# Performance work log

Measured on AMD Instinct MI355X. Metric: run time of the kernel, lower is better.

## Reference

```python
import jax, jax.numpy as jnp
import numpy as np

B, T, C, H = 4, 2048, 1024, 16
HS = C // H          # 64
DFF = 4 * C          # 4096
EPS = 1e-5


def _layernorm(x, g, b):
    mu = jnp.mean(x, axis=-1, keepdims=True)
    var = jnp.mean(jnp.square(x - mu), axis=-1, keepdims=True)
    return (x - mu) * jax.lax.rsqrt(var + EPS) * g + b


def setup_inputs() -> dict:
    key = jax.random.key(0)
    ks = jax.random.split(key, 12)
    s = 0.02
    return {
        "x": jax.random.normal(ks[0], (B, T, C), jnp.float32),
        "Wq": jax.random.normal(ks[1], (H, C, HS), jnp.float32) * s,
        "Wk": jax.random.normal(ks[2], (H, C, HS), jnp.float32) * s,
        "Wv": jax.random.normal(ks[3], (H, C, HS), jnp.float32) * s,
        "Wproj": jax.random.normal(ks[4], (C, C), jnp.float32) * s,
        "bproj": jnp.zeros((C,), jnp.float32),
        "ln1_g": jnp.ones((C,), jnp.float32),
        "ln1_b": jnp.zeros((C,), jnp.float32),
        "ln2_g": jnp.ones((C,), jnp.float32),
        "ln2_b": jnp.zeros((C,), jnp.float32),
        "W1": jax.random.normal(ks[5], (C, DFF), jnp.float32) * s,
        "b1": jnp.zeros((DFF,), jnp.float32),
        "W2": jax.random.normal(ks[6], (DFF, C), jnp.float32) * s,
        "b2": jnp.zeros((C,), jnp.float32),
    }


def reference(x, Wq, Wk, Wv, Wproj, bproj, ln1_g, ln1_b, ln2_g, ln2_b, W1, b1, W2, b2):
    Tn = x.shape[1]
    Cn = x.shape[2]
    # --- self-attention on ln1(x) ---
    h = _layernorm(x, ln1_g, ln1_b)
    q = jnp.einsum('btc,hcd->bhtd', h, Wq)
    k = jnp.einsum('btc,hcd->bhtd', h, Wk)
    v = jnp.einsum('btc,hcd->bhtd', h, Wv)
    # NOTE: original scales by C**-0.5 (full embed dim), not head_size**-0.5
    scores = jnp.einsum('bhtd,bhsd->bhts', q, k) * (Cn ** -0.5)
    mask = jnp.tril(jnp.ones((Tn, Tn), dtype=bool))
    scores = jnp.where(mask, scores, jnp.float32(-jnp.inf))
    att = jax.nn.softmax(scores, axis=-1)
    o = jnp.einsum('bhts,bhsd->bhtd', att, v)          # [B,H,T,HS]
    o = o.transpose(0, 2, 1, 3).reshape(x.shape)       # concat heads -> [B,T,C]
    x = x + o @ Wproj + bproj
    # --- feed-forward on ln2(x) ---
    h2 = _layernorm(x, ln2_g, ln2_b)
    x = x + jax.nn.relu(h2 @ W1 + b1) @ W2 + b2
    return x
```

## Files before the change

### kernel.cpp

```cpp
#include <hip/hip_runtime.h>
#include <hip/hip_bf16.h>
#include <stdint.h>

typedef __attribute__((ext_vector_type(8))) __bf16 bf16x8;
typedef __attribute__((ext_vector_type(4))) __bf16 bf16x4;
typedef __attribute__((ext_vector_type(4))) float f32x4;
typedef __attribute__((ext_vector_type(16))) float f32x16;
typedef __attribute__((ext_vector_type(4))) unsigned int u32x4;

typedef const __attribute__((address_space(1))) void* gas_ptr;
typedef __attribute__((address_space(3))) void* las_ptr;

static __device__ __forceinline__ void gload_lds16(const void* g, void* l) {
  __builtin_amdgcn_global_load_lds((gas_ptr)g, (las_ptr)l, 16, 0, 0);
}

static __device__ __forceinline__ unsigned int cvt_pk(float lo, float hi) {
  unsigned int r;
  asm("v_cvt_pk_bf16_f32 %0, %1, %2" : "=v"(r) : "v"(lo), "v"(hi));
  return r;
}

static __device__ __forceinline__ bf16x8 pack_frag(unsigned int a, unsigned int b,
                                                   unsigned int c, unsigned int d) {
  u32x4 t = {a, b, c, d};
  return __builtin_bit_cast(bf16x8, t);
}

static __device__ __forceinline__ void vm4() {
  asm volatile("s_waitcnt vmcnt(4)" ::: "memory");
}
static __device__ __forceinline__ void vm0() {
  asm volatile("s_waitcnt vmcnt(0)" ::: "memory");
}
static __device__ __forceinline__ void lgkm0sb() {
  asm volatile("s_waitcnt lgkmcnt(0)" ::: "memory");
  __builtin_amdgcn_sched_barrier(0);
}
static __device__ __forceinline__ void bar() {
  asm volatile("" ::: "memory");
  __builtin_amdgcn_s_barrier();
  asm volatile("" ::: "memory");
}

__global__ void transpose_cvt(const float* __restrict__ in, __bf16* __restrict__ out,
                              int R, int S) {
  __shared__ float t[32][33];
  int tx = threadIdx.x, ty = threadIdx.y;
  int r0 = blockIdx.y * 32, s0 = blockIdx.x * 32;
#pragma unroll
  for (int i = 0; i < 4; ++i) {
    int r = r0 + ty + i * 8;
    if (r < R && (s0 + tx) < S) t[ty + i * 8][tx] = in[(size_t)r * S + s0 + tx];
  }
  __syncthreads();
#pragma unroll
  for (int i = 0; i < 4; ++i) {
    int s = s0 + ty + i * 8;
    if (s < S && (r0 + tx) < R) out[(size_t)s * R + r0 + tx] = (__bf16)t[tx][ty + i * 8];
  }
}

__global__ void qkv_repack(const float* __restrict__ Wq, const float* __restrict__ Wk,
                           const float* __restrict__ Wv, __bf16* __restrict__ outT) {
  __shared__ float t[32][33];
  int z = blockIdx.z, sel = z >> 4, h = z & 15;
  const float* in = (sel == 0 ? Wq : sel == 1 ? Wk : Wv) + (size_t)h * 1024 * 64;
  __bf16* out = outT + (size_t)(sel * 1024 + h * 64) * 1024;
  int tx = threadIdx.x, ty = threadIdx.y;
  int r0 = blockIdx.y * 32, s0 = blockIdx.x * 32;
#pragma unroll
  for (int i = 0; i < 4; ++i)
    t[ty + i * 8][tx] = in[(size_t)(r0 + ty + i * 8) * 64 + s0 + tx];
  __syncthreads();
#pragma unroll
  for (int i = 0; i < 4; ++i)
    out[(size_t)(s0 + ty + i * 8) * 1024 + r0 + tx] = (__bf16)t[tx][ty + i * 8];
}

__global__ __launch_bounds__(256) void ln_kernel(const float* __restrict__ x,
                                                 const float* __restrict__ g,
                                                 const float* __restrict__ b,
                                                 __bf16* __restrict__ out) {
  __shared__ float red[8];
  int row = blockIdx.x, tid = threadIdx.x;
  float4 v = ((const float4*)(x + (size_t)row * 1024))[tid];
  float s = v.x + v.y + v.z + v.w;
  float s2 = v.x * v.x + v.y * v.y + v.z * v.z + v.w * v.w;
#pragma unroll
  for (int m = 1; m < 64; m <<= 1) { s += __shfl_xor(s, m); s2 += __shfl_xor(s2, m); }
  if ((tid & 63) == 0) { red[tid >> 6] = s; red[4 + (tid >> 6)] = s2; }
  __syncthreads();
  s = red[0] + red[1] + red[2] + red[3];
  s2 = red[4] + red[5] + red[6] + red[7];
  float mu = s * (1.0f / 1024.0f);
  float var = s2 * (1.0f / 1024.0f) - mu * mu;
  float rs = rsqrtf(var + 1e-5f);
  float4 gg = ((const float4*)g)[tid];
  float4 bb = ((const float4*)b)[tid];
  bf16x4 o4;
  o4[0] = (__bf16)((v.x - mu) * rs * gg.x + bb.x);
  o4[1] = (__bf16)((v.y - mu) * rs * gg.y + bb.y);
  o4[2] = (__bf16)((v.z - mu) * rs * gg.z + bb.z);
  o4[3] = (__bf16)((v.w - mu) * rs * gg.w + bb.w);
  *(bf16x4*)(out + (size_t)row * 1024 + tid * 4) = o4;
}

__global__ __launch_bounds__(256) void ff2_reduce(float* __restrict__ out,
                                                  const __bf16* __restrict__ p0,
                                                  const __bf16* __restrict__ p1,
                                                  const float* __restrict__ b2) {
  int i = blockIdx.x * 256 + threadIdx.x;
  float4 v = ((const float4*)out)[i];
  bf16x4 a = ((const bf16x4*)p0)[i];
  bf16x4 b = ((const bf16x4*)p1)[i];
  float4 bb = ((const float4*)b2)[i & 255];
  v.x += (float)a[0] + (float)b[0] + bb.x;
  v.y += (float)a[1] + (float)b[1] + bb.y;
  v.z += (float)a[2] + (float)b[2] + bb.z;
  v.w += (float)a[3] + (float)b[3] + bb.w;
  ((float4*)out)[i] = v;
}

template <int EPI>
__global__ __launch_bounds__(512) void gemm256(const __bf16* __restrict__ A,
                                               const __bf16* __restrict__ Bt,
                                               void* __restrict__ Cout,
                                               const float* __restrict__ bias,
                                               const float* __restrict__ resid,
                                               __bf16* __restrict__ q_out,
                                               __bf16* __restrict__ k_out,
                                               __bf16* __restrict__ vt_out,
                                               int M, int N, int K, int NBN) {
  __shared__ __align__(16) char lds[65536];
  const int tid = threadIdx.x;
  const int l = tid & 63, w = tid >> 6;
  const int wm = w >> 2, wn = w & 3;
  const int lr = l & 15, lg = l >> 4;

  int nwg = gridDim.x;
  int cpx = nwg >> 3;
  int orig = blockIdx.x;
  int wgid = (orig & 7) * cpx + (orig >> 3);
  int bn = wgid % NBN, bm = wgid / NBN;
  int n0 = bn * 256, m0 = bm * 256;

  const int Kloop = K / (int)gridDim.z;
  const int NT = Kloop >> 5;
  const size_t K2 = (size_t)K * 2;
  const size_t koff = (size_t)blockIdx.z * Kloop * 2;

  const int srow = tid >> 2;
  const int sslot = (tid & 3) * 16;
  const char* aA = (const char*)A + (size_t)(m0 + srow) * K2 + koff + sslot;
  const char* aB = (const char*)Bt + (size_t)(n0 + srow) * K2 + koff + sslot;

  auto stage = [&](int bufi, int kt) {
    char* d = lds + bufi * 32768 + tid * 16;
    const char* sA = aA + (size_t)kt * 64;
    const char* sB = aB + (size_t)kt * 64;
    gload_lds16(sA, d);
    gload_lds16(sA + (size_t)128 * K2, d + 8192);
    gload_lds16(sB, d + 16384);
    gload_lds16(sB + (size_t)128 * K2, d + 24576);
  };

  const int arow0 = (wm * 128 + lr) * 64 + lg * 16;
  const int brow0 = 16384 + (wn * 64 + lr) * 64 + lg * 16;

  f32x4 acc[8][4];
#pragma unroll
  for (int mi = 0; mi < 8; ++mi)
#pragma unroll
    for (int ni = 0; ni < 4; ++ni)
#pragma unroll
      for (int e = 0; e < 4; ++e) acc[mi][ni][e] = 0.0f;

  stage(0, 0);

  for (int t = 0; t < NT; ++t) {
    if (t + 1 < NT) { stage((t + 1) & 1, t + 1); vm4(); }
    else vm0();
    bar();
    const char* buf = lds + (t & 1) * 32768;
    bf16x8 af[8], bfr[4];
#pragma unroll
    for (int i = 0; i < 8; ++i)
      af[i] = *(const bf16x8*)(buf + arow0 + i * 1024);
#pragma unroll
    for (int j = 0; j < 4; ++j)
      bfr[j] = *(const bf16x8*)(buf + brow0 + j * 1024);
    lgkm0sb();
    __builtin_amdgcn_s_setprio(1);
#pragma unroll
    for (int mi = 0; mi < 8; ++mi)
#pragma unroll
      for (int ni = 0; ni < 4; ++ni)
        acc[mi][ni] = __builtin_amdgcn_mfma_f32_16x16x32_bf16(af[mi], bfr[ni], acc[mi][ni], 0, 0, 0);
    __builtin_amdgcn_s_setprio(0);
    bar();
  }

#pragma unroll
  for (int mi = 0; mi < 8; ++mi) {
    int rowb = m0 + wm * 128 + mi * 16 + lg * 4;
#pragma unroll
    for (int e = 0; e < 4; ++e) {
      int row = rowb + e;
#pragma unroll
      for (int ni = 0; ni < 4; ++ni) {
        int col = n0 + wn * 64 + ni * 16 + lr;
        float v = acc[mi][ni][e];
        size_t idx = (size_t)row * N + col;
        if (EPI == 0) {
          ((__bf16*)Cout)[idx] = (__bf16)v;
        } else if (EPI == 2) {
          v += bias[col];
          ((__bf16*)Cout)[idx] = (__bf16)fmaxf(v, 0.0f);
        } else if (EPI == 5) {
          (blockIdx.z ? k_out : q_out)[idx] = (__bf16)v;
        } else {
          int b = row >> 11, t2 = row & 2047;
          int sel = col >> 10, cc = col & 1023, h = cc >> 6, d = cc & 63;
          int bh = b * 16 + h;
          __bf16 val = (__bf16)v;
          if (sel == 0)
            q_out[((size_t)bh * 64 + d) * 2048 + t2] = val;
          else if (sel == 1)
            k_out[((size_t)bh * 2048 + t2) * 64 + d] = val;
          else
            vt_out[((size_t)bh * 64 + d) * 2048 + t2] = val;
        }
      }
    }
  }
}

template <int EPI>
__global__ __launch_bounds__(256, 3) void gemm2p(const __bf16* __restrict__ A,
                                                 const __bf16* __restrict__ Bt,
                                                 void* __restrict__ Cout,
                                                 const float* __restrict__ bias,
                                                 const float* __restrict__ resid,
                                                 int M, int N, int K, int NBN) {
  __shared__ __align__(16) char lds[49152];
  const int tid = threadIdx.x;
  const int l = tid & 63, w = tid >> 6;
  const int lr = l & 15, lg = l >> 4;

  int nwg = gridDim.x;
  int cpx = nwg >> 3;
  int orig = blockIdx.x;
  int wgid = (orig & 7) * cpx + (orig >> 3);
  int bn = wgid % NBN, bm = wgid / NBN;
  int n0 = bn * 128, m0 = bm * 128;

  const int NT = K >> 5;
  const size_t K2 = (size_t)K * 2;

  const int srow = tid >> 2;
  const int sslot = ((tid & 3) ^ ((tid >> 4) & 3)) << 4;
  const char* aA = (const char*)A + (size_t)(m0 + srow) * K2 + sslot;
  const char* aB = (const char*)Bt + (size_t)(n0 + srow) * K2 + sslot;

  auto stage = [&](int bufi, int kt) {
    char* d = lds + bufi * 16384 + tid * 16;
    const char* sA = aA + (size_t)kt * 64;
    const char* sB = aB + (size_t)kt * 64;
    gload_lds16(sA, d);
    gload_lds16(sA + (size_t)64 * K2, d + 4096);
    gload_lds16(sB, d + 8192);
    gload_lds16(sB + (size_t)64 * K2, d + 12288);
  };

  const int arow0 = ((w >> 1) * 64 + lr) * 64;
  const int brow0 = ((w & 1) * 64 + lr) * 64;
  const int cs = ((lg ^ (lr >> 2)) & 3) << 4;

  f32x4 acc[4][4];
#pragma unroll
  for (int mi = 0; mi < 4; ++mi)
#pragma unroll
    for (int ni = 0; ni < 4; ++ni)
#pragma unroll
      for (int e = 0; e < 4; ++e) acc[mi][ni][e] = 0.0f;

  stage(0, 0);
  stage(1, NT > 1 ? 1 : 0);
  vm4();
  bar();

  for (int t = 0; t < NT; ++t) {
    if (t + 2 < NT) stage((t + 2) % 3, t + 2);
    const char* buf = lds + (t % 3) * 16384;
    bf16x8 af[4], bfr[4];
#pragma unroll
    for (int i = 0; i < 4; ++i)
      af[i] = *(const bf16x8*)(buf + arow0 + i * 1024 + cs);
#pragma unroll
    for (int i = 0; i < 4; ++i)
      bfr[i] = *(const bf16x8*)(buf + 8192 + brow0 + i * 1024 + cs);
    lgkm0sb();
    __builtin_amdgcn_s_setprio(1);
#pragma unroll
    for (int mi = 0; mi < 4; ++mi)
#pragma unroll
      for (int ni = 0; ni < 4; ++ni)
        acc[mi][ni] = __builtin_amdgcn_mfma_f32_16x16x32_bf16(af[mi], bfr[ni], acc[mi][ni], 0, 0, 0);
    __builtin_amdgcn_s_setprio(0);
    if (t + 2 < NT) vm4(); else vm0();
    bar();
  }

#pragma unroll
  for (int mi = 0; mi < 4; ++mi) {
    int rowb = m0 + (w >> 1) * 64 + mi * 16 + lg * 4;
#pragma unroll
    for (int e = 0; e < 4; ++e) {
      int row = rowb + e;
#pragma unroll
      for (int ni = 0; ni < 4; ++ni) {
        int col = n0 + (w & 1) * 64 + ni * 16 + lr;
        float v = acc[mi][ni][e];
        size_t idx = (size_t)row * N + col;
        if (EPI == 1) {
          ((float*)Cout)[idx] = resid[idx] + v + bias[col];
        } else {
          ((__bf16*)Cout)[idx] = (__bf16)v;
        }
      }
    }
  }
}

__global__ __launch_bounds__(256) void attn_kernel4(const __bf16* __restrict__ Qt,
                                                    const __bf16* __restrict__ Kh,
                                                    const __bf16* __restrict__ Vt,
                                                    __bf16* __restrict__ o) {
  __shared__ __align__(16) char Klds[16384];
  __shared__ __align__(16) char Vlds[16384];
  int tid = threadIdx.x;
  int l = tid & 63, w = tid >> 6;
  int lq = l & 31, hi = l >> 5;
  int p = blockIdx.x, bh = blockIdx.y;
  int b = bh >> 4, h = bh & 15;

  const char* Kbase = (const char*)(Kh + (size_t)bh * 2048 * 64);
  const char* Vbase = (const char*)(Vt + (size_t)bh * 64 * 2048);
  const __bf16* Qbase = Qt + (size_t)bh * 64 * 2048;
  __bf16* Obase = o + (size_t)b * 2048 * 1024 + h * 64;

  int srow = tid >> 3;
  int schunk = (tid & 7) * 16;
  int sw0 = (srow & 7) << 4;
  int swz = (lq & 7) << 4;

  auto stageKV = [&](int bufi, int s0) {
    char* kd = Klds + bufi * 8192 + tid * 16;
    char* vd = Vlds + bufi * 8192 + tid * 16;
    gload_lds16(Kbase + (size_t)(s0 + srow) * 128 + (schunk ^ sw0), kd);
    gload_lds16(Kbase + (size_t)(s0 + srow + 32) * 128 + (schunk ^ sw0), kd + 4096);
    gload_lds16(Vbase + (size_t)srow * 4096 + s0 * 2 + (schunk ^ sw0), vd);
    gload_lds16(Vbase + (size_t)(srow + 32) * 4096 + s0 * 2 + (schunk ^ sw0), vd + 4096);
  };

  for (int sweep = 0; sweep < 2; ++sweep) {
    int t = (sweep == 0) ? p : 15 - p;
    int qw = t * 128 + w * 32;
    int qglob = qw + lq;

    bf16x8 qb[4];
    const __bf16* qsrc = Qbase + (size_t)(hi * 8) * 2048 + qw + lq;
#pragma unroll
    for (int s = 0; s < 4; ++s)
#pragma unroll
      for (int j = 0; j < 8; ++j)
        qb[s][j] = qsrc[(size_t)(s * 16 + j) * 2048];

    f32x16 oacc0, oacc1;
#pragma unroll
    for (int i = 0; i < 16; ++i) { oacc0[i] = 0.0f; oacc1[i] = 0.0f; }
    float m_q = -3.0e38f, l_q = 0.0f;

    int nkb = 2 * t + 2;
    stageKV(0, 0);
    for (int kb = 0; kb < nkb; ++kb) {
      int s0 = kb * 64;
      if (kb + 1 < nkb) { stageKV((kb + 1) & 1, s0 + 64); vm4(); }
      else vm0();
      bar();
      const char* Kb = Klds + (kb & 1) * 8192;
      const char* Vb = Vlds + (kb & 1) * 8192;

      if (s0 <= qw + 31) {
        f32x16 st0, st1;
#pragma unroll
        for (int i = 0; i < 16; ++i) { st0[i] = 0.0f; st1[i] = 0.0f; }
#pragma unroll
        for (int s = 0; s < 4; ++s) {
          bf16x8 ka = *(const bf16x8*)(Kb + lq * 128 + ((s * 32 + hi * 16) ^ swz));
          st0 = __builtin_amdgcn_mfma_f32_32x32x16_bf16(ka, qb[s], st0, 0, 0, 0);
        }
#pragma unroll
        for (int s = 0; s < 4; ++s) {
          bf16x8 ka = *(const bf16x8*)(Kb + (32 + lq) * 128 + ((s * 32 + hi * 16) ^ swz));
          st1 = __builtin_amdgcn_mfma_f32_32x32x16_bf16(ka, qb[s], st1, 0, 0, 0);
        }
        if (s0 + 63 > qw) {
#pragma unroll
          for (int r = 0; r < 16; ++r) {
            int key0 = s0 + (r & 3) + 8 * (r >> 2) + 4 * hi;
            if (key0 > qglob) st0[r] = -1.0e38f;
            if (key0 + 32 > qglob) st1[r] = -1.0e38f;
          }
        }
        float mx8[8];
#pragma unroll
        for (int i = 0; i < 8; ++i)
          mx8[i] = fmaxf(fmaxf(st0[i], st0[i + 8]), fmaxf(st1[i], st1[i + 8]));
        float mx = fmaxf(fmaxf(fmaxf(mx8[0], mx8[1]), fmaxf(mx8[2], mx8[3])),
                         fmaxf(fmaxf(mx8[4], mx8[5]), fmaxf(mx8[6], mx8[7])));
        {
          float u = mx, v = mx;
          asm("v_permlane32_swap_b32 %0, %1" : "+v"(u), "+v"(v));
          mx = fmaxf(u, v);
        }
        float mt_s = mx * 0.03125f;
        if (__any(mt_s > m_q + 8.0f)) {
          float mnew = fmaxf(m_q, mt_s);
          float scv = exp2f((m_q - mnew) * 1.44269504f);
          m_q = mnew;
          l_q *= scv;
#pragma unroll
          for (int r = 0; r < 16; ++r) {
            int qr = (r & 3) + 8 * (r >> 2) + 4 * hi;
            float scO = __shfl(scv, qr);
            oacc0[r] *= scO;
            oacc1[r] *= scO;
          }
        }
        float m2 = m_q * 1.44269504f;
#pragma unroll
        for (int r = 0; r < 16; ++r) {
          st0[r] = exp2f(fmaf(st0[r], 0.045084389f, -m2));
          st1[r] = exp2f(fmaf(st1[r], 0.045084389f, -m2));
        }
        float s8[8];
#pragma unroll
        for (int i = 0; i < 8; ++i)
          s8[i] = (st0[i] + st0[i + 8]) + (st1[i] + st1[i + 8]);
        float ps = ((s8[0] + s8[1]) + (s8[2] + s8[3])) +
                   ((s8[4] + s8[5]) + (s8[6] + s8[7]));
        {
          float u = ps, v = ps;
          asm("v_permlane32_swap_b32 %0, %1" : "+v"(u), "+v"(v));
          ps = u + v;
        }
        l_q += ps;

        {
          unsigned int w0 = cvt_pk(st0[0], st0[1]), w1 = cvt_pk(st0[2], st0[3]);
          unsigned int w2 = cvt_pk(st0[4], st0[5]), w3 = cvt_pk(st0[6], st0[7]);
          asm("v_permlane32_swap_b32 %0, %1" : "+v"(w0), "+v"(w2));
          asm("v_permlane32_swap_b32 %0, %1" : "+v"(w1), "+v"(w3));
          bf16x8 pa0 = pack_frag(w0, w1, w2, w3);
          unsigned int w4 = cvt_pk(st0[8], st0[9]), w5 = cvt_pk(st0[10], st0[11]);
          unsigned int w6 = cvt_pk(st0[12], st0[13]), w7 = cvt_pk(st0[14], st0[15]);
          asm("v_permlane32_swap_b32 %0, %1" : "+v"(w4), "+v"(w6));
          asm("v_permlane32_swap_b32 %0, %1" : "+v"(w5), "+v"(w7));
          bf16x8 pa1 = pack_frag(w4, w5, w6, w7);
          bf16x8 v00 = *(const bf16x8*)(Vb + lq * 128 + ((hi * 16) ^ swz));
          bf16x8 v01 = *(const bf16x8*)(Vb + (32 + lq) * 128 + ((hi * 16) ^ swz));
          bf16x8 v10 = *(const bf16x8*)(Vb + lq * 128 + ((32 + hi * 16) ^ swz));
          bf16x8 v11 = *(const bf16x8*)(Vb + (32 + lq) * 128 + ((32 + hi * 16) ^ swz));
          oacc0 = __builtin_amdgcn_mfma_f32_32x32x16_bf16(pa0, v00, oacc0, 0, 0, 0);
          oacc1 = __builtin_amdgcn_mfma_f32_32x32x16_bf16(pa0, v01, oacc1, 0, 0, 0);
          oacc0 = __builtin_amdgcn_mfma_f32_32x32x16_bf16(pa1, v10, oacc0, 0, 0, 0);
          oacc1 = __builtin_amdgcn_mfma_f32_32x32x16_bf16(pa1, v11, oacc1, 0, 0, 0);
        }
        {
          unsigned int w0 = cvt_pk(st1[0], st1[1]), w1 = cvt_pk(st1[2], st1[3]);
          unsigned int w2 = cvt_pk(st1[4], st1[5]), w3 = cvt_pk(st1[6], st1[7]);
          asm("v_permlane32_swap_b32 %0, %1" : "+v"(w0), "+v"(w2));
          asm("v_permlane32_swap_b32 %0, %1" : "+v"(w1), "+v"(w3));
          bf16x8 pa0 = pack_frag(w0, w1, w2, w3);
          unsigned int w4 = cvt_pk(st1[8], st1[9]), w5 = cvt_pk(st1[10], st1[11]);
          unsigned int w6 = cvt_pk(st1[12], st1[13]), w7 = cvt_pk(st1[14], st1[15]);
          asm("v_permlane32_swap_b32 %0, %1" : "+v"(w4), "+v"(w6));
          asm("v_permlane32_swap_b32 %0, %1" : "+v"(w5), "+v"(w7));
          bf16x8 pa1 = pack_frag(w4, w5, w6, w7);
          bf16x8 v00 = *(const bf16x8*)(Vb + lq * 128 + ((64 + hi * 16) ^ swz));
          bf16x8 v01 = *(const bf16x8*)(Vb + (32 + lq) * 128 + ((64 + hi * 16) ^ swz));
          bf16x8 v10 = *(const bf16x8*)(Vb + lq * 128 + ((96 + hi * 16) ^ swz));
          bf16x8 v11 = *(const bf16x8*)(Vb + (32 + lq) * 128 + ((96 + hi * 16) ^ swz));
          oacc0 = __builtin_amdgcn_mfma_f32_32x32x16_bf16(pa0, v00, oacc0, 0, 0, 0);
          oacc1 = __builtin_amdgcn_mfma_f32_32x32x16_bf16(pa0, v01, oacc1, 0, 0, 0);
          oacc0 = __builtin_amdgcn_mfma_f32_32x32x16_bf16(pa1, v10, oacc0, 0, 0, 0);
          oacc1 = __builtin_amdgcn_mfma_f32_32x32x16_bf16(pa1, v11, oacc1, 0, 0, 0);
        }
      }
      bar();
    }
#pragma unroll
    for (int r = 0; r < 16; ++r) {
      int qr = (r & 3) + 8 * (r >> 2) + 4 * hi;
      float linv = 1.0f / __shfl(l_q, qr);
      size_t row = qw + qr;
      Obase[row * 1024 + lq] = (__bf16)(oacc0[r] * linv);
      Obase[row * 1024 + 32 + lq] = (__bf16)(oacc1[r] * linv);
    }
  }
}

extern "C" void kernel_launch(void* const* d_in, const int* in_sizes, int n_in,
                              void* d_out, int out_size, void* d_ws, size_t ws_size,
                              hipStream_t stream) {
  const float* x     = (const float*)d_in[0];
  const float* Wq    = (const float*)d_in[1];
  const float* Wk    = (const float*)d_in[2];
  const float* Wv    = (const float*)d_in[3];
  const float* Wproj = (const float*)d_in[4];
  const float* bproj = (const float*)d_in[5];
  const float* ln1_g = (const float*)d_in[6];
  const float* ln1_b = (const float*)d_in[7];
  const float* ln2_g = (const float*)d_in[8];
  const float* ln2_b = (const float*)d_in[9];
  const float* W1    = (const float*)d_in[10];
  const float* b1    = (const float*)d_in[11];
  const float* W2    = (const float*)d_in[12];
  const float* b2    = (const float*)d_in[13];
  float* out = (float*)d_out;

  char* ws = (char*)d_ws;
  __bf16* actA   = (__bf16*)(ws + 0);
  __bf16* WqkvT  = (__bf16*)(ws + 16777216);
  __bf16* WprojT = (__bf16*)(ws + 23068672);
  __bf16* W1T    = (__bf16*)(ws + 25165824);
  __bf16* W2T    = (__bf16*)(ws + 33554432);
  __bf16* Qt     = (__bf16*)(ws + 41943040);
  __bf16* Kh     = (__bf16*)(ws + 58720256);
  __bf16* Vt     = (__bf16*)(ws + 75497472);
  __bf16* obuf   = (__bf16*)(ws + 92274688);
  __bf16* ff1    = Qt;
  __bf16* p0     = (__bf16*)(ws + 0);
  __bf16* p1     = (__bf16*)(ws + 16777216);

  dim3 t32x8(32, 8);
  qkv_repack<<<dim3(2, 32, 48), t32x8, 0, stream>>>(Wq, Wk, Wv, WqkvT);
  transpose_cvt<<<dim3(32, 32), t32x8, 0, stream>>>(Wproj, WprojT, 1024, 1024);
  transpose_cvt<<<dim3(128, 32), t32x8, 0, stream>>>(W1, W1T, 1024, 4096);
  transpose_cvt<<<dim3(32, 128), t32x8, 0, stream>>>(W2, W2T, 4096, 1024);

  ln_kernel<<<8192, 256, 0, stream>>>(x, ln1_g, ln1_b, actA);
  gemm256<4><<<dim3(384, 1, 1), 512, 0, stream>>>(actA, WqkvT, nullptr, nullptr, nullptr,
                                                  Qt, Kh, Vt, 8192, 3072, 1024, 12);
  attn_kernel4<<<dim3(8, 64), 256, 0, stream>>>(Qt, Kh, Vt, obuf);
  gemm2p<1><<<dim3(512, 1, 1), 256, 0, stream>>>(obuf, WprojT, out, bproj, x,
                                                 8192, 1024, 1024, 8);
  ln_kernel<<<8192, 256, 0, stream>>>(out, ln2_g, ln2_b, actA);
  gemm256<2><<<dim3(512, 1, 1), 512, 0, stream>>>(actA, W1T, ff1, b1, nullptr,
                                                  nullptr, nullptr, nullptr, 8192, 4096, 1024, 16);
  gemm256<5><<<dim3(128, 1, 2), 512, 0, stream>>>(ff1, W2T, nullptr, nullptr, nullptr,
                                                  p0, p1, nullptr, 8192, 1024, 4096, 4);
  ff2_reduce<<<8192, 256, 0, stream>>>(out, p0, p1, b2);
}
```

Baseline: 431.0 us.

## Replace 256x256 GEMM with 8-phase pipelined kernel using swizzled 128KB LDS

Rewrites the main bf16 GEMM (QKV, FF1, FF2) into an 8-wave kernel with a K-tile of 64 instead of 32. LDS grows to 128KB, split into two buffers. Each tile is cut into four quadrant phases, and global-to-LDS loads for later tiles are interleaved between MFMA phases under barriers and vmcnt waits. LDS rows are XOR-swizzled to avoid bank conflicts, and the wave-to-output mapping changes to quadrant-strided rows and columns. The goal is to hide memory latency and LDS stalls behind MFMA work, at the cost of more barriers, more LDS use limiting occupancy, and redundant clamped loads on the last tiles.

After: 394.5 us. -8.5%, faster.

```diff
diff --git a/kernel.cpp b/kernel.cpp
--- a/kernel.cpp
+++ b/kernel.cpp
@@ -29,6 +29,9 @@
 
 static __device__ __forceinline__ void vm4() {
   asm volatile("s_waitcnt vmcnt(4)" ::: "memory");
+}
+static __device__ __forceinline__ void vm6() {
+  asm volatile("s_waitcnt vmcnt(6)" ::: "memory");
 }
 static __device__ __forceinline__ void vm0() {
   asm volatile("s_waitcnt vmcnt(0)" ::: "memory");
@@ -123,16 +126,16 @@
 }
 
 template <int EPI>
-__global__ __launch_bounds__(512) void gemm256(const __bf16* __restrict__ A,
-                                               const __bf16* __restrict__ Bt,
-                                               void* __restrict__ Cout,
-                                               const float* __restrict__ bias,
-                                               const float* __restrict__ resid,
-                                               __bf16* __restrict__ q_out,
-                                               __bf16* __restrict__ k_out,
-                                               __bf16* __restrict__ vt_out,
-                                               int M, int N, int K, int NBN) {
-  __shared__ __align__(16) char lds[65536];
+__global__ __launch_bounds__(512) void gemm8p(const __bf16* __restrict__ A,
+                                              const __bf16* __restrict__ Bt,
+                                              void* __restrict__ Cout,
+                                              const float* __restrict__ bias,
+                                              const float* __restrict__ resid,
+                                              __bf16* __restrict__ q_out,
+                                              __bf16* __restrict__ k_out,
+                                              __bf16* __restrict__ vt_out,
+                                              int M, int N, int K, int NBN) {
+  __shared__ __align__(16) char lds[131072];
   const int tid = threadIdx.x;
   const int l = tid & 63, w = tid >> 6;
   const int wm = w >> 2, wn = w & 3;
@@ -146,27 +149,32 @@
   int n0 = bn * 256, m0 = bm * 256;
 
   const int Kloop = K / (int)gridDim.z;
-  const int NT = Kloop >> 5;
+  const int NT = Kloop >> 6;
   const size_t K2 = (size_t)K * 2;
   const size_t koff = (size_t)blockIdx.z * Kloop * 2;
 
-  const int srow = tid >> 2;
-  const int sslot = (tid & 3) * 16;
-  const char* aA = (const char*)A + (size_t)(m0 + srow) * K2 + koff + sslot;
-  const char* aB = (const char*)Bt + (size_t)(n0 + srow) * K2 + koff + sslot;
-
-  auto stage = [&](int bufi, int kt) {
-    char* d = lds + bufi * 32768 + tid * 16;
-    const char* sA = aA + (size_t)kt * 64;
-    const char* sB = aB + (size_t)kt * 64;
-    gload_lds16(sA, d);
-    gload_lds16(sA + (size_t)128 * K2, d + 8192);
-    gload_lds16(sB, d + 16384);
-    gload_lds16(sB + (size_t)128 * K2, d + 24576);
-  };
-
-  const int arow0 = (wm * 128 + lr) * 64 + lg * 16;
-  const int brow0 = 16384 + (wn * 64 + lr) * 64 + lg * 16;
+  const int srow = tid >> 3, slot = tid & 7;
+  const int sswz = (slot ^ (srow & 7)) << 4;
+  const char* aA = (const char*)A + (size_t)(m0 + srow) * K2 + koff + sswz;
+  const char* aB = (const char*)Bt + (size_t)(n0 + srow) * K2 + koff + sswz;
+
+  auto stageA = [&](char* buf, int half, int kt) {
+    char* d = buf + half * 16384 + tid * 16;
+    const char* s = aA + (size_t)(half * 128) * K2 + (size_t)kt * 128;
+    gload_lds16(s, d);
+    gload_lds16(s + (size_t)64 * K2, d + 8192);
+  };
+  auto stageB = [&](char* buf, int half, int kt) {
+    char* d = buf + 32768 + half * 16384 + tid * 16;
+    const char* s = aB + (size_t)(half * 128) * K2 + (size_t)kt * 128;
+    gload_lds16(s, d);
+    gload_lds16(s + (size_t)64 * K2, d + 8192);
+  };
+
+  const int arow = (wm * 64 + lr) * 128;
+  const int brow = (wn * 32 + lr) * 128;
+  const int ck0 = ((lg) ^ (lr & 7)) << 4;
+  const int ck1 = ((4 + lg) ^ (lr & 7)) << 4;
 
   f32x4 acc[8][4];
 #pragma unroll
@@ -176,44 +184,94 @@
 #pragma unroll
       for (int e = 0; e < 4; ++e) acc[mi][ni][e] = 0.0f;
 
-  stage(0, 0);
-
-  for (int t = 0; t < NT; ++t) {
-    if (t + 1 < NT) { stage((t + 1) & 1, t + 1); vm4(); }
-    else vm0();
+  bf16x8 af[4][2], b0f[2][2], b1f[2][2];
+
+  auto ldsA = [&](const char* buf, int mh) {
+#pragma unroll
+    for (int i = 0; i < 4; ++i) {
+      const char* p = buf + mh * 16384 + arow + i * 2048;
+      af[i][0] = *(const bf16x8*)(p + ck0);
+      af[i][1] = *(const bf16x8*)(p + ck1);
+    }
+  };
+  auto ldsB = [&](bf16x8 (&dst)[2][2], const char* buf, int nh) {
+#pragma unroll
+    for (int j = 0; j < 2; ++j) {
+      const char* p = buf + 32768 + nh * 16384 + brow + j * 2048;
+      dst[j][0] = *(const bf16x8*)(p + ck0);
+      dst[j][1] = *(const bf16x8*)(p + ck1);
+    }
+  };
+  auto mmq = [&](int mh, bf16x8 (&bf)[2][2], int nh) {
+    __builtin_amdgcn_s_setprio(1);
+#pragma unroll
+    for (int i = 0; i < 4; ++i)
+#pragma unroll
+      for (int j = 0; j < 2; ++j) {
+        int mi = mh * 4 + i, ni = nh * 2 + j;
+        acc[mi][ni] = __builtin_amdgcn_mfma_f32_16x16x32_bf16(af[i][0], bf[j][0], acc[mi][ni], 0, 0, 0);
+        acc[mi][ni] = __builtin_amdgcn_mfma_f32_16x16x32_bf16(af[i][1], bf[j][1], acc[mi][ni], 0, 0, 0);
+      }
+    __builtin_amdgcn_s_setprio(0);
+  };
+
+  char* bufE = lds;
+  char* bufO = lds + 65536;
+
+  stageA(bufE, 0, 0);
+  stageB(bufE, 0, 0);
+  stageB(bufE, 1, 0);
+  stageA(bufE, 1, 0);
+  if (NT > 1) { stageA(bufO, 0, 1); stageB(bufO, 0, 1); }
+  else        { stageA(bufO, 0, 0); stageB(bufO, 0, 0); }
+  vm4();
+  bar();
+
+  auto do_tile = [&](char* cur, char* oth, int t) {
+    int kN = (t + 1 < NT) ? t + 1 : NT - 1;
+    int kN2 = (t + 2 < NT) ? t + 2 : NT - 1;
+    ldsA(cur, 0);
+    ldsB(b0f, cur, 0);
+    stageB(oth, 1, kN);
+    vm6(); bar(); lgkm0sb();
+    mmq(0, b0f, 0);
     bar();
-    const char* buf = lds + (t & 1) * 32768;
-    bf16x8 af[8], bfr[4];
-#pragma unroll
-    for (int i = 0; i < 8; ++i)
-      af[i] = *(const bf16x8*)(buf + arow0 + i * 1024);
-#pragma unroll
-    for (int j = 0; j < 4; ++j)
-      bfr[j] = *(const bf16x8*)(buf + brow0 + j * 1024);
-    lgkm0sb();
-    __builtin_amdgcn_s_setprio(1);
-#pragma unroll
-    for (int mi = 0; mi < 8; ++mi)
-#pragma unroll
-      for (int ni = 0; ni < 4; ++ni)
-        acc[mi][ni] = __builtin_amdgcn_mfma_f32_16x16x32_bf16(af[mi], bfr[ni], acc[mi][ni], 0, 0, 0);
-    __builtin_amdgcn_s_setprio(0);
+    ldsB(b1f, cur, 1);
+    stageA(oth, 1, kN);
+    vm6(); bar(); lgkm0sb();
+    mmq(0, b1f, 1);
     bar();
+    ldsA(cur, 1);
+    stageA(cur, 0, kN2);
+    vm6(); bar(); lgkm0sb();
+    mmq(1, b1f, 1);
+    bar();
+    stageB(cur, 0, kN2);
+    vm6(); bar();
+    mmq(1, b0f, 0);
+    bar();
+  };
+
+  for (int t = 0; t < NT; t += 2) {
+    do_tile(bufE, bufO, t);
+    do_tile(bufO, bufE, t + 1);
   }
 
 #pragma unroll
   for (int mi = 0; mi < 8; ++mi) {
-    int rowb = m0 + wm * 128 + mi * 16 + lg * 4;
+    int rowb = m0 + (mi >> 2) * 128 + wm * 64 + (mi & 3) * 16 + lg * 4;
 #pragma unroll
     for (int e = 0; e < 4; ++e) {
       int row = rowb + e;
 #pragma unroll
       for (int ni = 0; ni < 4; ++ni) {
-        int col = n0 + wn * 64 + ni * 16 + lr;
+        int col = n0 + (ni >> 1) * 128 + wn * 32 + (ni & 1) * 16 + lr;
         float v = acc[mi][ni][e];
         size_t idx = (size_t)row * N + col;
         if (EPI == 0) {
           ((__bf16*)Cout)[idx] = (__bf16)v;
+        } else if (EPI == 1) {
+          ((float*)Cout)[idx] = resid[idx] + v + bias[col];
         } else if (EPI == 2) {
           v += bias[col];
           ((__bf16*)Cout)[idx] = (__bf16)fmaxf(v, 0.0f);
@@ -552,15 +610,15 @@
   transpose_cvt<<<dim3(32, 128), t32x8, 0, stream>>>(W2, W2T, 4096, 1024);
 
   ln_kernel<<<8192, 256, 0, stream>>>(x, ln1_g, ln1_b, actA);
-  gemm256<4><<<dim3(384, 1, 1), 512, 0, stream>>>(actA, WqkvT, nullptr, nullptr, nullptr,
-                                                  Qt, Kh, Vt, 8192, 3072, 1024, 12);
+  gemm8p<4><<<dim3(384, 1, 1), 512, 0, stream>>>(actA, WqkvT, nullptr, nullptr, nullptr,
+                                                 Qt, Kh, Vt, 8192, 3072, 1024, 12);
   attn_kernel4<<<dim3(8, 64), 256, 0, stream>>>(Qt, Kh, Vt, obuf);
   gemm2p<1><<<dim3(512, 1, 1), 256, 0, stream>>>(obuf, WprojT, out, bproj, x,
                                                  8192, 1024, 1024, 8);
   ln_kernel<<<8192, 256, 0, stream>>>(out, ln2_g, ln2_b, actA);
-  gemm256<2><<<dim3(512, 1, 1), 512, 0, stream>>>(actA, W1T, ff1, b1, nullptr,
-                                                  nullptr, nullptr, nullptr, 8192, 4096, 1024, 16);
-  gemm256<5><<<dim3(128, 1, 2), 512, 0, stream>>>(ff1, W2T, nullptr, nullptr, nullptr,
-                                                  p0, p1, nullptr, 8192, 1024, 4096, 4);
+  gemm8p<2><<<dim3(512, 1, 1), 512, 0, stream>>>(actA, W1T, ff1, b1, nullptr,
+                                                 nullptr, nullptr, nullptr, 8192, 4096, 1024, 16);
+  gemm8p<5><<<dim3(128, 1, 2), 512, 0, stream>>>(ff1, W2T, nullptr, nullptr, nullptr,
+                                                 p0, p1, nullptr, 8192, 1024, 4096, 4);
   ff2_reduce<<<8192, 256, 0, stream>>>(out, p0, p1, b2);
 }
```
